# Optimization experiments

Hardware: AMD Instinct MI355X
Metric: run time of the kernel (lower is better)

## Reference

```python
import jax, jax.numpy as jnp
import numpy as np

TEMP = 0.2
NUM_PATCH, BATCH, DIM = 16, 512, 2048


def _l2_normalize(x, axis=-1, eps=1e-12):
    # matches torch F.normalize: x / max(||x||, eps)
    norm = jnp.linalg.norm(x, axis=axis, keepdims=True)
    return x / jnp.maximum(norm, eps)


def setup_inputs() -> dict:
    key = jax.random.key(0)
    features = jax.random.normal(key, (NUM_PATCH, BATCH, DIM), dtype=jnp.float32)
    return {"features": features}


def reference(features) -> jnp.ndarray:
    P, B, D = features.shape
    # z_avg: mean over the num_patch crops -> [B, D]
    z_avg = _l2_normalize(features.mean(axis=0), axis=1)
    # concat crops along batch -> [P*B, D], then L2 normalize rows
    f = _l2_normalize(features.reshape(P * B, D), axis=1)
    # similarity matrix [P*B, B]
    sim = f @ z_avg.T
    # labels = identity(B) tiled P times along rows => positive of row i is column i % B.
    # CE with target 0 after concat([pos, negs]) == -pos/T + logsumexp(all/T)
    rows = jnp.arange(P * B)
    pos = sim[rows, rows % B]
    logits = sim / TEMP
    loss = jnp.mean(jax.nn.logsumexp(logits, axis=1) - pos / TEMP)
    return loss
```

## Files before the change

kernel.cpp:

```cpp
#include <hip/hip_runtime.h>
#include <hip/hip_bf16.h>
#include <math.h>

#define NP 16
#define NB 512
#define ND 2048
#define NM (NP*NB)
#define BM 64
#define BN 128
#define BK 64
#define NS (ND/BK)
#define NCB (NB/BN)

typedef __attribute__((ext_vector_type(4))) float f32x4;
typedef unsigned int u32;

__device__ inline float dot4(float4 v) {
    return v.x * v.x + v.y * v.y + v.z * v.z + v.w * v.w;
}

#if __has_builtin(__builtin_amdgcn_cvt_pk_fp8_f32)
__device__ inline u32 pack4_fp8(float a, float b, float c, float d) {
    int w = 0;
    w = __builtin_amdgcn_cvt_pk_fp8_f32(a, b, w, false);
    w = __builtin_amdgcn_cvt_pk_fp8_f32(c, d, w, true);
    return (u32)w;
}
#else
#include <hip/hip_fp8.h>
__device__ inline u32 pack4_fp8(float a, float b, float c, float d) {
    u32 w  = (u32)__hip_cvt_float_to_fp8(a, __HIP_SATFINITE, __HIP_E4M3);
    w |= (u32)__hip_cvt_float_to_fp8(b, __HIP_SATFINITE, __HIP_E4M3) << 8;
    w |= (u32)__hip_cvt_float_to_fp8(c, __HIP_SATFINITE, __HIP_E4M3) << 16;
    w |= (u32)__hip_cvt_float_to_fp8(d, __HIP_SATFINITE, __HIP_E4M3) << 24;
    return w;
}
#endif

__global__ __launch_bounds__(512) void prep_kernel(
        const float* __restrict__ feat,
        unsigned char* __restrict__ an,
        unsigned char* __restrict__ zn,
        float* __restrict__ accg, u32* __restrict__ cntr) {
    const int b = blockIdx.x, tid = threadIdx.x;
    const int lane = tid & 63, wv = tid >> 6;
    if (b == 0 && tid == 0) { accg[0] = 0.f; cntr[0] = 0u; }

    const int dbase = wv * 256 + lane * 4;
    const float4* fp4 = (const float4*)feat;

    float4 rv[16];
    float4 z = make_float4(0.f, 0.f, 0.f, 0.f);
#pragma unroll
    for (int p = 0; p < NP; ++p) {
        rv[p] = fp4[((size_t)(p * NB + b) * ND + dbase) >> 2];
        z.x += rv[p].x; z.y += rv[p].y; z.z += rv[p].z; z.w += rv[p].w;
    }

    __shared__ float sm_ssq[NP][8];
    __shared__ float sm_z[8];
    __shared__ float sm_inv[NP + 1];
#pragma unroll
    for (int p = 0; p < NP; ++p) {
        float ss = dot4(rv[p]);
#pragma unroll
        for (int off = 32; off > 0; off >>= 1) ss += __shfl_xor(ss, off);
        if (lane == 0) sm_ssq[p][wv] = ss;
    }
    {
        float zs = dot4(z);
#pragma unroll
        for (int off = 32; off > 0; off >>= 1) zs += __shfl_xor(zs, off);
        if (lane == 0) sm_z[wv] = zs;
    }
    __syncthreads();
    if (tid < NP) {
        float t = 0.f;
#pragma unroll
        for (int v = 0; v < 8; ++v) t += sm_ssq[tid][v];
        sm_inv[tid] = 1.f / fmaxf(sqrtf(t), 1e-12f);
    } else if (tid == NP) {
        float t = 0.f;
#pragma unroll
        for (int v = 0; v < 8; ++v) t += sm_z[v];
        sm_inv[NP] = 1.f / fmaxf(sqrtf(t), 1e-12f);
    }
    __syncthreads();

#pragma unroll
    for (int p = 0; p < NP; ++p) {
        const float inv = sm_inv[p];
        ((u32*)(an + (size_t)(p * NB + b) * ND))[dbase >> 2] =
            pack4_fp8(rv[p].x * inv, rv[p].y * inv, rv[p].z * inv, rv[p].w * inv);
    }
    const float iz = sm_inv[NP];
    ((u32*)(zn + (size_t)b * ND))[dbase >> 2] =
        pack4_fp8(z.x * iz, z.y * iz, z.z * iz, z.w * iz);
}

__global__ __launch_bounds__(256, 2) void gemm_loss_kernel(
        const unsigned char* __restrict__ an,
        const unsigned char* __restrict__ zn,
        float* __restrict__ psum_g,
        float* __restrict__ ppos_g) {
    __shared__ __align__(16) unsigned char abuf[3 * BM * BK];
    __shared__ __align__(16) unsigned char bbuf[3 * BN * BK];
    __shared__ float sm_sum[BM][2];
    __shared__ float sm_pos[BM];

    const int tid  = threadIdx.x;
    const int lane = tid & 63;
    const int w    = tid >> 6;
    const int wr   = w >> 1;
    const int wc   = w & 1;
    const int l15  = lane & 15;
    const int l4   = lane >> 4;
    const int xcd    = blockIdx.x & 7;
    const int slot   = blockIdx.x >> 3;
    const int cb     = slot & 3;
    const int rowblk = xcd + 8 * (slot >> 2);
    const int brow = rowblk * BM;
    const int bcol = cb * BN;

    f32x4 acc[2][4] = {};

    const int sra = tid >> 2;
    const int sca = (tid & 3) ^ ((sra >> 2) & 3);
    const unsigned char* asrc = an + (size_t)(brow + sra) * ND + sca * 16;
    const unsigned char* bsrc0;
    const unsigned char* bsrc1;
    {
        int q0 = tid, q1 = 256 + tid;
        int r0 = q0 >> 2, c0 = (q0 & 3) ^ ((r0 >> 2) & 3);
        int r1 = q1 >> 2, c1 = (q1 & 3) ^ ((r1 >> 2) & 3);
        bsrc0 = zn + (size_t)(bcol + r0) * ND + c0 * 16;
        bsrc1 = zn + (size_t)(bcol + r1) * ND + c1 * 16;
    }

#define STAGE(BI, S) do {                                                     \
        const int koB_ = (S) * BK;                                            \
        __builtin_amdgcn_global_load_lds((const u32*)(asrc + koB_),           \
            (u32*)(&abuf[(BI) * 4096 + tid * 16]), 16, 0, 0);                 \
        __builtin_amdgcn_global_load_lds((const u32*)(bsrc0 + koB_),          \
            (u32*)(&bbuf[(BI) * 8192 + tid * 16]), 16, 0, 0);                 \
        __builtin_amdgcn_global_load_lds((const u32*)(bsrc1 + koB_),          \
            (u32*)(&bbuf[(BI) * 8192 + 4096 + tid * 16]), 16, 0, 0);          \
    } while (0)

    STAGE(0, 0);
    STAGE(1, 1);

    int acur = 0, astg = 2;
    for (int s = 0; s < NS; ++s) {
        if (s + 1 < NS) asm volatile("s_waitcnt vmcnt(3)" ::: "memory");
        else            asm volatile("s_waitcnt vmcnt(0)" ::: "memory");
        __builtin_amdgcn_sched_barrier(0);
        __builtin_amdgcn_s_barrier();
        __builtin_amdgcn_sched_barrier(0);

        long long af[2][2], bf[2][4];
#pragma unroll
        for (int kc = 0; kc < 2; ++kc) {
            const int kk = kc * 4 + l4;
#pragma unroll
            for (int m = 0; m < 2; ++m) {
                int r = wr * 32 + m * 16 + l15;
                int g = (kk >> 1) ^ ((r >> 2) & 3);
                af[kc][m] = *(const long long*)(
                    &abuf[acur * 4096 + r * 64 + g * 16 + (kk & 1) * 8]);
            }
#pragma unroll
            for (int n = 0; n < 4; ++n) {
                int r = wc * 64 + n * 16 + l15;
                int g = (kk >> 1) ^ ((r >> 2) & 3);
                bf[kc][n] = *(const long long*)(
                    &bbuf[acur * 8192 + r * 64 + g * 16 + (kk & 1) * 8]);
            }
        }

        if (s + 2 < NS) STAGE(astg, s + 2);

        __builtin_amdgcn_s_setprio(1);
#pragma unroll
        for (int kc = 0; kc < 2; ++kc)
#pragma unroll
        for (int m = 0; m < 2; ++m)
#pragma unroll
        for (int n = 0; n < 4; ++n)
            acc[m][n] = __builtin_amdgcn_mfma_f32_16x16x32_fp8_fp8(
                af[kc][m], bf[kc][n], acc[m][n], 0, 0, 0);
        __builtin_amdgcn_s_setprio(0);

        acur = (acur == 2) ? 0 : acur + 1;
        astg = (astg == 2) ? 0 : astg + 1;
    }
#undef STAGE

#pragma unroll
    for (int m = 0; m < 2; ++m) {
#pragma unroll
        for (int r = 0; r < 4; ++r) {
            const int lrow = wr * 32 + m * 16 + l4 * 4 + r;
            float lg[4];
            float se = 0.f;
#pragma unroll
            for (int n = 0; n < 4; ++n) {
                lg[n] = acc[m][n][r] * 5.0f;
                se += __expf(lg[n]);
            }
            se += __shfl_xor(se, 1);
            se += __shfl_xor(se, 2);
            se += __shfl_xor(se, 4);
            se += __shfl_xor(se, 8);
            if (l15 == 0) sm_sum[lrow][wc] = se;
            const int posc = (brow + lrow) & (NB - 1);
#pragma unroll
            for (int n = 0; n < 4; ++n)
                if (bcol + wc * 64 + n * 16 + l15 == posc) sm_pos[lrow] = lg[n];
        }
    }
    __syncthreads();

    if (tid < BM) {
        const int lrow = tid;
        const int grow = brow + lrow;
        psum_g[cb * NM + grow] = sm_sum[lrow][0] + sm_sum[lrow][1];
        if (((grow & (NB - 1)) >> 7) == cb) ppos_g[grow] = sm_pos[lrow];
    }
}

__global__ __launch_bounds__(256) void reduce_kernel(
        const float* __restrict__ psum_g, const float* __restrict__ ppos_g,
        float* __restrict__ acc_g, u32* __restrict__ counter,
        float* __restrict__ out) {
    const int row = blockIdx.x * 256 + threadIdx.x;
    float tot = psum_g[row] + psum_g[NM + row]
              + psum_g[2 * NM + row] + psum_g[3 * NM + row];
    float term = __logf(tot) - ppos_g[row];
#pragma unroll
    for (int off = 32; off > 0; off >>= 1) term += __shfl_xor(term, off);
    __shared__ float wsum[4];
    const int lane = threadIdx.x & 63, wv = threadIdx.x >> 6;
    if (lane == 0) wsum[wv] = term;
    __syncthreads();
    if (threadIdx.x == 0) {
        atomicAdd(acc_g, wsum[0] + wsum[1] + wsum[2] + wsum[3]);
        __threadfence();
        u32 old = atomicAdd(counter, 1u);
        if (old == 31u) {
            float total = atomicAdd(acc_g, 0.0f);
            out[0] = total * (1.0f / (float)NM);
        }
    }
}

extern "C" void kernel_launch(void* const* d_in, const int* in_sizes, int n_in,
                              void* d_out, int out_size, void* d_ws, size_t ws_size,
                              hipStream_t stream) {
    const float* feat = (const float*)d_in[0];

    unsigned char* an = (unsigned char*)d_ws;
    unsigned char* zn = an + (size_t)NM * ND;
    float* psum = (float*)(zn + (size_t)NB * ND);
    float* ppos = psum + NCB * NM;
    float* accg = ppos + NM;
    u32*   cntr = (u32*)(accg + 1);

    prep_kernel<<<NB, 512, 0, stream>>>(feat, an, zn, accg, cntr);
    gemm_loss_kernel<<<(NM / BM) * NCB, 256, 0, stream>>>(an, zn, psum, ppos);
    reduce_kernel<<<NM / 256, 256, 0, stream>>>(psum, ppos, accg, cntr,
                                                (float*)d_out);
}
```

Measured before the change: 44.51 us.

## Double the FP8 GEMM K-tile to 128 and widen the LDS swizzle

Raises the K step of the FP8 MFMA similarity GEMM from 64 to 128 bytes. This halves the number of pipeline iterations and block barriers, and puts more MFMAs between waits. The global-to-LDS load mapping is rewritten to match: 8 threads per row, an XOR swizzle over 8 16-byte chunks, two A loads and four B loads per stage, and the vmcnt wait threshold raised to fit. The triple-buffered LDS footprint roughly doubles. That may lower occupancy, and it only works if the shared buffers are sized from BK.

```diff
diff --git a/kernel.cpp b/kernel.cpp
--- a/kernel.cpp
+++ b/kernel.cpp
@@ -8,7 +8,7 @@
 #define NM (NP*NB)
 #define BM 64
 #define BN 128
-#define BK 64
+#define BK 128
 #define NS (ND/BK)
 #define NCB (NB/BN)
 
@@ -124,27 +124,23 @@
 
     f32x4 acc[2][4] = {};
 
-    const int sra = tid >> 2;
-    const int sca = (tid & 3) ^ ((sra >> 2) & 3);
-    const unsigned char* asrc = an + (size_t)(brow + sra) * ND + sca * 16;
-    const unsigned char* bsrc0;
-    const unsigned char* bsrc1;
-    {
-        int q0 = tid, q1 = 256 + tid;
-        int r0 = q0 >> 2, c0 = (q0 & 3) ^ ((r0 >> 2) & 3);
-        int r1 = q1 >> 2, c1 = (q1 & 3) ^ ((r1 >> 2) & 3);
-        bsrc0 = zn + (size_t)(bcol + r0) * ND + c0 * 16;
-        bsrc1 = zn + (size_t)(bcol + r1) * ND + c1 * 16;
-    }
+    const int sr  = tid >> 3;
+    const int scs = (tid & 7) ^ (sr & 7);
+    const unsigned char* asrc = an + (size_t)(brow + sr) * ND + scs * 16;
+    const unsigned char* bsrc = zn + (size_t)(bcol + sr) * ND + scs * 16;
 
 #define STAGE(BI, S) do {                                                     \
         const int koB_ = (S) * BK;                                            \
         __builtin_amdgcn_global_load_lds((const u32*)(asrc + koB_),           \
-            (u32*)(&abuf[(BI) * 4096 + tid * 16]), 16, 0, 0);                 \
-        __builtin_amdgcn_global_load_lds((const u32*)(bsrc0 + koB_),          \
-            (u32*)(&bbuf[(BI) * 8192 + tid * 16]), 16, 0, 0);                 \
-        __builtin_amdgcn_global_load_lds((const u32*)(bsrc1 + koB_),          \
-            (u32*)(&bbuf[(BI) * 8192 + 4096 + tid * 16]), 16, 0, 0);          \
+            (u32*)(&abuf[(BI) * 8192 + tid * 16]), 16, 0, 0);                 \
+        __builtin_amdgcn_global_load_lds((const u32*)(asrc + 32 * ND + koB_), \
+            (u32*)(&abuf[(BI) * 8192 + 4096 + tid * 16]), 16, 0, 0);          \
+        _Pragma("unroll")                                                     \
+        for (int i = 0; i < 4; ++i) {                                         \
+            __builtin_amdgcn_global_load_lds(                                 \
+                (const u32*)(bsrc + (size_t)(32 * i) * ND + koB_),            \
+                (u32*)(&bbuf[(BI) * 16384 + i * 4096 + tid * 16]), 16, 0, 0); \
+        }                                                                     \
     } while (0)
 
     STAGE(0, 0);
@@ -152,29 +148,30 @@
 
     int acur = 0, astg = 2;
     for (int s = 0; s < NS; ++s) {
-        if (s + 1 < NS) asm volatile("s_waitcnt vmcnt(3)" ::: "memory");
+        if (s + 1 < NS) asm volatile("s_waitcnt vmcnt(6)" ::: "memory");
         else            asm volatile("s_waitcnt vmcnt(0)" ::: "memory");
         __builtin_amdgcn_sched_barrier(0);
         __builtin_amdgcn_s_barrier();
         __builtin_amdgcn_sched_barrier(0);
 
-        long long af[2][2], bf[2][4];
-#pragma unroll
-        for (int kc = 0; kc < 2; ++kc) {
-            const int kk = kc * 4 + l4;
+        long long af[4][2], bf[4][4];
+#pragma unroll
+        for (int kc = 0; kc < 4; ++kc) {
+            const int g16 = kc * 2 + (l4 >> 1);
+            const int lo8 = (l4 & 1) * 8;
 #pragma unroll
             for (int m = 0; m < 2; ++m) {
                 int r = wr * 32 + m * 16 + l15;
-                int g = (kk >> 1) ^ ((r >> 2) & 3);
+                int g = g16 ^ (r & 7);
                 af[kc][m] = *(const long long*)(
-                    &abuf[acur * 4096 + r * 64 + g * 16 + (kk & 1) * 8]);
+                    &abuf[acur * 8192 + r * BK + g * 16 + lo8]);
             }
 #pragma unroll
             for (int n = 0; n < 4; ++n) {
                 int r = wc * 64 + n * 16 + l15;
-                int g = (kk >> 1) ^ ((r >> 2) & 3);
+                int g = g16 ^ (r & 7);
                 bf[kc][n] = *(const long long*)(
-                    &bbuf[acur * 8192 + r * 64 + g * 16 + (kk & 1) * 8]);
+                    &bbuf[acur * 16384 + r * BK + g * 16 + lo8]);
             }
         }
 
@@ -182,7 +179,7 @@
 
         __builtin_amdgcn_s_setprio(1);
 #pragma unroll
-        for (int kc = 0; kc < 2; ++kc)
+        for (int kc = 0; kc < 4; ++kc)
 #pragma unroll
         for (int m = 0; m < 2; ++m)
 #pragma unroll
```

Result: faster. 43.35 us, median of 2 (-2.6%).
